# Kernel tuning notes

Hardware: AMD Instinct MI355X
Metric: run time of the kernel (lower is better)

## Reference

```python
import jax, jax.numpy as jnp
import numpy as np

B, T, C, H = 16, 2048, 192, 64

def setup_inputs() -> dict:
    key = jax.random.key(0)
    k1, k2, k3, k4 = jax.random.split(key, 4)
    x = jax.random.normal(k1, (B, T, C), dtype=jnp.float32)
    Wq = jax.random.normal(k2, (C, H), dtype=jnp.float32) * (C ** -0.5)
    Wk = jax.random.normal(k3, (C, H), dtype=jnp.float32) * (C ** -0.5)
    Wv = jax.random.normal(k4, (C, H), dtype=jnp.float32) * (C ** -0.5)
    return {"x": x, "Wq": Wq, "Wk": Wk, "Wv": Wv}

def reference(x, Wq, Wk, Wv):
    # One head of causal self-attention (dropout in eval mode / identity).
    q = x @ Wq                       # [B, T, H]
    k = x @ Wk                       # [B, T, H]
    v = x @ Wv                       # [B, T, H]
    scale = q.shape[-1] ** -0.5
    wei = jnp.einsum('bth,bsh->bts', q, k) * scale   # [B, T, T]
    t = wei.shape[-1]
    causal = jnp.tril(jnp.ones((t, t), dtype=bool))  # tril mask
    wei = jnp.where(causal, wei, -jnp.inf)
    wei = jax.nn.softmax(wei, axis=-1)
    out = jnp.einsum('bts,bsh->bth', wei, v)         # [B, T, H]
    return out
```

## Files before the change

kernel.cpp:

```cpp
#include <hip/hip_runtime.h>

#define B 16
#define T 2048
#define C 192
#define H 64

typedef __bf16 bf16x8 __attribute__((ext_vector_type(8)));
typedef __bf16 bf16x4 __attribute__((ext_vector_type(4)));
typedef float  f32x4  __attribute__((ext_vector_type(4)));

#define MFMA(a, b, c) __builtin_amdgcn_mfma_f32_16x16x32_bf16(a, b, c, 0, 0, 0)

#define SM_BIAS 24.0f

__global__ __launch_bounds__(512) void qkv_mfma_kernel(
    const float* __restrict__ x,
    const float* __restrict__ Wq, const float* __restrict__ Wk,
    const float* __restrict__ Wv,
    __bf16* __restrict__ qb, __bf16* __restrict__ kb, __bf16* __restrict__ vt)
{
    __shared__ __bf16 Ws[192][200];
    __shared__ __bf16 tile[128][72];

    const int tid  = threadIdx.x;
    const int w    = tid >> 6;
    const int lid  = tid & 15;
    const int quad = (tid & 63) >> 4;
    const int m0   = blockIdx.x * 128 + w * 16;

    #pragma unroll
    for (int i = 0; i < 18; i++) {
        const int p = i * 512 + tid;
        const int m = p / 3072;
        const int r = p - m * 3072;
        const int k = r >> 4;
        const int nc4 = (r & 15) << 2;
        const float* W = (m == 0) ? Wq : (m == 1) ? Wk : Wv;
        const float4 v = *(const float4*)(W + k * H + nc4);
        const int n = m * 64 + nc4;
        Ws[n + 0][k] = (__bf16)v.x;
        Ws[n + 1][k] = (__bf16)v.y;
        Ws[n + 2][k] = (__bf16)v.z;
        Ws[n + 3][k] = (__bf16)v.w;
    }

    const float* xrow = x + (size_t)(m0 + lid) * C + quad * 8;
    bf16x8 af[6];
    #pragma unroll
    for (int kc = 0; kc < 6; kc++) {
        const float4 a0 = *(const float4*)(xrow + kc * 32);
        const float4 a1 = *(const float4*)(xrow + kc * 32 + 4);
        af[kc][0] = (__bf16)a0.x; af[kc][1] = (__bf16)a0.y;
        af[kc][2] = (__bf16)a0.z; af[kc][3] = (__bf16)a0.w;
        af[kc][4] = (__bf16)a1.x; af[kc][5] = (__bf16)a1.y;
        af[kc][6] = (__bf16)a1.z; af[kc][7] = (__bf16)a1.w;
    }
    __syncthreads();

    f32x4 acc[12] = {};
    #pragma unroll
    for (int kc = 0; kc < 6; kc++)
        #pragma unroll
        for (int nt = 0; nt < 12; nt++) {
            const bf16x8 bfr =
                *(const bf16x8*)&Ws[nt * 16 + lid][kc * 32 + quad * 8];
            acc[nt] = MFMA(af[kc], bfr, acc[nt]);
        }

    #pragma unroll
    for (int nt = 0; nt < 8; nt++) {
        const int n = nt * 16 + lid;
        __bf16* dst = (n < 64) ? qb : kb;
        const int col = n & 63;
        const float scale = (n < 64) ? 0.1803368801111204f : 1.0f;
        #pragma unroll
        for (int r = 0; r < 4; r++) {
            const int row = m0 + quad * 4 + r;
            dst[(size_t)row * H + col] = (__bf16)(acc[nt][r] * scale);
        }
    }

    #pragma unroll
    for (int nt = 8; nt < 12; nt++) {
        const int col = (nt - 8) * 16 + lid;
        #pragma unroll
        for (int r = 0; r < 4; r++)
            tile[w * 16 + quad * 4 + r][col] = (__bf16)(acc[nt][r]);
    }
    __syncthreads();

    const int bb = blockIdx.x >> 4;
    const int t0 = (blockIdx.x & 15) << 7;
    #pragma unroll
    for (int it = 0; it < 2; ++it) {
        const int q   = it * 512 + tid;
        const int h   = q >> 4;
        const int tl0 = (q & 15) * 8;
        bf16x8 d;
        #pragma unroll
        for (int j = 0; j < 8; j++) d[j] = tile[tl0 + j][h];
        *(bf16x8*)(vt + ((size_t)(bb * H + h)) * T + t0 + tl0) = d;
    }
}

__global__ __launch_bounds__(512, 2) void attn_kernel(
    const __bf16* __restrict__ qb,
    const __bf16* __restrict__ kb,
    const __bf16* __restrict__ vt,
    float* __restrict__ out)
{
    __shared__ __bf16 Kb[2][2][64][72];
    __shared__ __bf16 Vb[2][2][64][68];

    const int tid  = threadIdx.x;
    const int wv   = tid >> 6;
    const int grp  = wv >> 2;
    const int w    = wv & 3;
    const int lid  = tid & 15;
    const int quad = (tid & 63) >> 4;

    const int b   = blockIdx.x & 15;
    const int pr  = blockIdx.x >> 4;
    const int qtH = 31 - pr, qtL = pr;
    const int nchH = qtH + 1;
    const int ntot = 33;
    const size_t bbase = (size_t)b * T;

    const int qH = (qtH << 6) + w * 16;
    const int qL = (qtL << 6) + w * 16;

    const __bf16* qrH = qb + (bbase + qH + lid) * H + quad * 8;
    const bf16x8 qfH0 = *(const bf16x8*)(qrH);
    const bf16x8 qfH1 = *(const bf16x8*)(qrH + 32);
    const __bf16* qrL = qb + (bbase + qL + lid) * H + quad * 8;
    const bf16x8 qfL0 = *(const bf16x8*)(qrL);
    const bf16x8 qfL1 = *(const bf16x8*)(qrL + 32);

    const __bf16* kgb = kb + bbase * H;
    const __bf16* vgb = vt + (size_t)b * H * T;

    const int ra = tid >> 3, ca = (tid & 7) * 8;

    auto keyof = [&](int i) {
        if (i > ntot - 1) i = ntot - 1;
        return (i < nchH ? i : i - nchH) << 6;
    };

    bf16x8 kr[2], vr2[2];
    auto prefetch = [&](int s) {
        #pragma unroll
        for (int g = 0; g < 2; g++) {
            const int key0 = keyof(2 * s + g);
            kr[g]  = *(const bf16x8*)(kgb + (size_t)(key0 + ra) * H + ca);
            vr2[g] = *(const bf16x8*)(vgb + (size_t)ra * T + key0 + ca);
        }
    };

    f32x4 OH[4] = {}, OL[4] = {};
    float lsH = 0.f, lsL = 0.f;

    auto doChunk = [&](f32x4 (&O)[4], float& ls, bf16x8 cq0, bf16x8 cq1,
                       int cqw, int key0, int cur) {
        const __bf16 (*Kc)[72] = Kb[cur][grp];
        const __bf16 (*Vc)[68] = Vb[cur][grp];
        bf16x8 kf[8];
        #pragma unroll
        for (int j = 0; j < 4; j++) {
            kf[2*j]   = *(const bf16x8*)&Kc[j * 16 + lid][quad * 8];
            kf[2*j+1] = *(const bf16x8*)&Kc[j * 16 + lid][32 + quad * 8];
        }
        bf16x8 bv0[4], bv1[4];
        #pragma unroll
        for (int ht = 0; ht < 4; ht++) {
            const __bf16* vr_ = &Vc[ht * 16 + lid][quad * 4];
            ((bf16x4*)&bv0[ht])[0] = *(const bf16x4*)(vr_);
            ((bf16x4*)&bv0[ht])[1] = *(const bf16x4*)(vr_ + 16);
            ((bf16x4*)&bv1[ht])[0] = *(const bf16x4*)(vr_ + 32);
            ((bf16x4*)&bv1[ht])[1] = *(const bf16x4*)(vr_ + 48);
        }
        bf16x8 af0, af1;
        const bool boundary = (key0 + 63 > cqw);
        #pragma unroll
        for (int j = 0; j < 4; j++) {
            f32x4 sS = {-SM_BIAS, -SM_BIAS, -SM_BIAS, -SM_BIAS};
            sS = MFMA(kf[2*j], cq0, sS);
            sS = MFMA(kf[2*j+1], cq1, sS);
            if (boundary) {
                #pragma unroll
                for (int r = 0; r < 4; r++)
                    if (key0 + j * 16 + quad * 4 + r > cqw + lid) sS[r] = -1e30f;
            }
            #pragma unroll
            for (int r = 0; r < 4; r++) {
                const float p = __builtin_amdgcn_exp2f(sS[r]);
                ls += p;
                if      (j == 0) af0[r]     = (__bf16)p;
                else if (j == 1) af0[4 + r] = (__bf16)p;
                else if (j == 2) af1[r]     = (__bf16)p;
                else             af1[4 + r] = (__bf16)p;
            }
        }
        #pragma unroll
        for (int ht = 0; ht < 4; ht++) {
            O[ht] = MFMA(af0, bv0[ht], O[ht]);
            O[ht] = MFMA(af1, bv1[ht], O[ht]);
        }
    };

    prefetch(0);
    int cur = 0;
    for (int s = 0; s < 17; s++) {
        *(bf16x8*)&Kb[cur][0][ra][ca] = kr[0];
        *(bf16x8*)&Kb[cur][1][ra][ca] = kr[1];
        *(bf16x8*)&Vb[cur][0][ra][ca] = vr2[0];
        *(bf16x8*)&Vb[cur][1][ra][ca] = vr2[1];
        __syncthreads();
        if (s + 1 < 17) prefetch(s + 1);

        const int i = 2 * s + grp;
        if (i < ntot) {
            const bool heavy = (i < nchH);
            const int key0 = (heavy ? i : i - nchH) << 6;
            if (heavy) doChunk(OH, lsH, qfH0, qfH1, qH, key0, cur);
            else       doChunk(OL, lsL, qfL0, qfL1, qL, key0, cur);
        }
        cur ^= 1;
    }

    __syncthreads();
    float* sO = (float*)&Kb[0][0][0][0];
    float* sL = (float*)&Vb[0][0][0][0];

    float lh = lsH; lh += __shfl_xor(lh, 16, 64); lh += __shfl_xor(lh, 32, 64);
    float ll = lsL; ll += __shfl_xor(ll, 16, 64); ll += __shfl_xor(ll, 32, 64);

    if (grp == 1) {
        #pragma unroll
        for (int ht = 0; ht < 4; ht++)
            #pragma unroll
            for (int r = 0; r < 4; r++) {
                sO[((0 * 4 + w) * 16 + quad * 4 + r) * 64 + ht * 16 + lid] = OH[ht][r];
                sO[((1 * 4 + w) * 16 + quad * 4 + r) * 64 + ht * 16 + lid] = OL[ht][r];
            }
        if ((tid & 63) < 16) {
            sL[(0 * 4 + w) * 16 + lid] = lh;
            sL[(1 * 4 + w) * 16 + lid] = ll;
        }
    }
    __syncthreads();
    if (grp == 0) {
        lh += sL[(0 * 4 + w) * 16 + lid];
        ll += sL[(1 * 4 + w) * 16 + lid];
        #pragma unroll
        for (int ht = 0; ht < 4; ht++)
            #pragma unroll
            for (int r = 0; r < 4; r++) {
                const float LrH = __shfl(lh, quad * 4 + r, 16);
                const float vH = OH[ht][r]
                    + sO[((0 * 4 + w) * 16 + quad * 4 + r) * 64 + ht * 16 + lid];
                out[(bbase + qH + quad * 4 + r) * H + ht * 16 + lid] = vH / LrH;

                const float LrL = __shfl(ll, quad * 4 + r, 16);
                const float vL = OL[ht][r]
                    + sO[((1 * 4 + w) * 16 + quad * 4 + r) * 64 + ht * 16 + lid];
                out[(bbase + qL + quad * 4 + r) * H + ht * 16 + lid] = vL / LrL;
            }
    }
}

extern "C" void kernel_launch(void* const* d_in, const int* in_sizes, int n_in,
                              void* d_out, int out_size, void* d_ws, size_t ws_size,
                              hipStream_t stream)
{
    const float* x  = (const float*)d_in[0];
    const float* Wq = (const float*)d_in[1];
    const float* Wk = (const float*)d_in[2];
    const float* Wv = (const float*)d_in[3];

    const size_t BTH = (size_t)B * T * H;
    __bf16* qbuf = (__bf16*)d_ws;
    __bf16* kbuf = qbuf + BTH;
    __bf16* vtb  = kbuf + BTH;
    float* outp = (float*)d_out;

    qkv_mfma_kernel<<<B * T / 128, 512, 0, stream>>>(x, Wq, Wk, Wv,
                                                     qbuf, kbuf, vtb);
    attn_kernel<<<B * T / 128, 512, 0, stream>>>(qbuf, kbuf, vtb, outp);
}
```

Before: 103.8 us.

## Split attention block into four key-groups with two query tiles per wave

Each workgroup now has four wave-groups that each process a different key chunk per step, instead of two. Every wave handles 32 query rows (two 16-row tiles), so each K/V fragment read from LDS feeds twice as many MFMAs. This halves the number of pipeline steps and barriers and cuts LDS read traffic per FLOP. In exchange it uses double the LDS and more registers for accumulators, which may lower occupancy, and the final cross-group reduction through shared memory is larger.

```diff
diff --git a/kernel.cpp b/kernel.cpp
--- a/kernel.cpp
+++ b/kernel.cpp
@@ -103,19 +103,21 @@
     }
 }
 
+#define KB_E (64 * 72)
+#define VB_E (64 * 68)
+
 __global__ __launch_bounds__(512, 2) void attn_kernel(
     const __bf16* __restrict__ qb,
     const __bf16* __restrict__ kb,
     const __bf16* __restrict__ vt,
     float* __restrict__ out)
 {
-    __shared__ __bf16 Kb[2][2][64][72];
-    __shared__ __bf16 Vb[2][2][64][68];
+    __shared__ __align__(16) __bf16 smem[8 * KB_E + 8 * VB_E];
 
     const int tid  = threadIdx.x;
     const int wv   = tid >> 6;
-    const int grp  = wv >> 2;
-    const int w    = wv & 3;
+    const int grp  = wv >> 1;
+    const int w2   = wv & 1;
     const int lid  = tid & 15;
     const int quad = (tid & 63) >> 4;
 
@@ -124,146 +126,188 @@
     const int qtH = 31 - pr, qtL = pr;
     const int nchH = qtH + 1;
     const int ntot = 33;
+    const int nsteps = 9;
     const size_t bbase = (size_t)b * T;
 
-    const int qH = (qtH << 6) + w * 16;
-    const int qL = (qtL << 6) + w * 16;
-
-    const __bf16* qrH = qb + (bbase + qH + lid) * H + quad * 8;
-    const bf16x8 qfH0 = *(const bf16x8*)(qrH);
-    const bf16x8 qfH1 = *(const bf16x8*)(qrH + 32);
-    const __bf16* qrL = qb + (bbase + qL + lid) * H + quad * 8;
-    const bf16x8 qfL0 = *(const bf16x8*)(qrL);
-    const bf16x8 qfL1 = *(const bf16x8*)(qrL + 32);
+    const int qHb = (qtH << 6) + w2 * 32;
+    const int qLb = (qtL << 6) + w2 * 32;
+
+    const __bf16* qp;
+    qp = qb + (bbase + qHb + lid) * H + quad * 8;
+    const bf16x8 qfHa0 = *(const bf16x8*)(qp);
+    const bf16x8 qfHa1 = *(const bf16x8*)(qp + 32);
+    qp = qb + (bbase + qHb + 16 + lid) * H + quad * 8;
+    const bf16x8 qfHb0 = *(const bf16x8*)(qp);
+    const bf16x8 qfHb1 = *(const bf16x8*)(qp + 32);
+    qp = qb + (bbase + qLb + lid) * H + quad * 8;
+    const bf16x8 qfLa0 = *(const bf16x8*)(qp);
+    const bf16x8 qfLa1 = *(const bf16x8*)(qp + 32);
+    qp = qb + (bbase + qLb + 16 + lid) * H + quad * 8;
+    const bf16x8 qfLb0 = *(const bf16x8*)(qp);
+    const bf16x8 qfLb1 = *(const bf16x8*)(qp + 32);
 
     const __bf16* kgb = kb + bbase * H;
     const __bf16* vgb = vt + (size_t)b * H * T;
 
-    const int ra = tid >> 3, ca = (tid & 7) * 8;
+    const int gq = tid >> 7;
+    const int tt = tid & 127;
 
     auto keyof = [&](int i) {
         if (i > ntot - 1) i = ntot - 1;
         return (i < nchH ? i : i - nchH) << 6;
     };
 
-    bf16x8 kr[2], vr2[2];
+    bf16x8 kr[4], vrr[4];
     auto prefetch = [&](int s) {
-        #pragma unroll
-        for (int g = 0; g < 2; g++) {
-            const int key0 = keyof(2 * s + g);
-            kr[g]  = *(const bf16x8*)(kgb + (size_t)(key0 + ra) * H + ca);
-            vr2[g] = *(const bf16x8*)(vgb + (size_t)ra * T + key0 + ca);
+        const int key0 = keyof(4 * s + gq);
+        #pragma unroll
+        for (int i = 0; i < 4; i++) {
+            const int p = i * 128 + tt, r = p >> 3, c = (p & 7) * 8;
+            kr[i]  = *(const bf16x8*)(kgb + (size_t)(key0 + r) * H + c);
+            vrr[i] = *(const bf16x8*)(vgb + (size_t)r * T + key0 + c);
         }
     };
 
-    f32x4 OH[4] = {}, OL[4] = {};
-    float lsH = 0.f, lsL = 0.f;
-
-    auto doChunk = [&](f32x4 (&O)[4], float& ls, bf16x8 cq0, bf16x8 cq1,
-                       int cqw, int key0, int cur) {
-        const __bf16 (*Kc)[72] = Kb[cur][grp];
-        const __bf16 (*Vc)[68] = Vb[cur][grp];
-        bf16x8 kf[8];
+    f32x4 OHa[4] = {}, OHb[4] = {}, OLa[4] = {}, OLb[4] = {};
+    float lsHa = 0.f, lsHb = 0.f, lsLa = 0.f, lsLb = 0.f;
+
+    auto doChunk = [&](f32x4 (&OA)[4], f32x4 (&OB)[4], float& lA, float& lB,
+                       bf16x8 qa0, bf16x8 qa1, bf16x8 qb0_, bf16x8 qb1_,
+                       int qbase, int key0, int cur) {
+        const __bf16 (*Kc)[72] =
+            (const __bf16(*)[72])(smem + (cur * 4 + grp) * KB_E);
+        const __bf16 (*Vc)[68] =
+            (const __bf16(*)[68])(smem + 8 * KB_E + (cur * 4 + grp) * VB_E);
+        bf16x8 afa0, afa1, afb0, afb1;
+        const bool boundary = (key0 + 63 > qbase);
         #pragma unroll
         for (int j = 0; j < 4; j++) {
-            kf[2*j]   = *(const bf16x8*)&Kc[j * 16 + lid][quad * 8];
-            kf[2*j+1] = *(const bf16x8*)&Kc[j * 16 + lid][32 + quad * 8];
-        }
-        bf16x8 bv0[4], bv1[4];
-        #pragma unroll
-        for (int ht = 0; ht < 4; ht++) {
-            const __bf16* vr_ = &Vc[ht * 16 + lid][quad * 4];
-            ((bf16x4*)&bv0[ht])[0] = *(const bf16x4*)(vr_);
-            ((bf16x4*)&bv0[ht])[1] = *(const bf16x4*)(vr_ + 16);
-            ((bf16x4*)&bv1[ht])[0] = *(const bf16x4*)(vr_ + 32);
-            ((bf16x4*)&bv1[ht])[1] = *(const bf16x4*)(vr_ + 48);
-        }
-        bf16x8 af0, af1;
-        const bool boundary = (key0 + 63 > cqw);
-        #pragma unroll
-        for (int j = 0; j < 4; j++) {
-            f32x4 sS = {-SM_BIAS, -SM_BIAS, -SM_BIAS, -SM_BIAS};
-            sS = MFMA(kf[2*j], cq0, sS);
-            sS = MFMA(kf[2*j+1], cq1, sS);
+            const bf16x8 k0 = *(const bf16x8*)&Kc[j * 16 + lid][quad * 8];
+            const bf16x8 k1 = *(const bf16x8*)&Kc[j * 16 + lid][32 + quad * 8];
+            f32x4 sa = {-SM_BIAS, -SM_BIAS, -SM_BIAS, -SM_BIAS};
+            f32x4 sb = sa;
+            sa = MFMA(k0, qa0, sa);  sa = MFMA(k1, qa1, sa);
+            sb = MFMA(k0, qb0_, sb); sb = MFMA(k1, qb1_, sb);
             if (boundary) {
                 #pragma unroll
-                for (int r = 0; r < 4; r++)
-                    if (key0 + j * 16 + quad * 4 + r > cqw + lid) sS[r] = -1e30f;
+                for (int r = 0; r < 4; r++) {
+                    const int key = key0 + j * 16 + quad * 4 + r;
+                    if (key > qbase + lid)      sa[r] = -1e30f;
+                    if (key > qbase + 16 + lid) sb[r] = -1e30f;
+                }
             }
             #pragma unroll
             for (int r = 0; r < 4; r++) {
-                const float p = __builtin_amdgcn_exp2f(sS[r]);
-                ls += p;
-                if      (j == 0) af0[r]     = (__bf16)p;
-                else if (j == 1) af0[4 + r] = (__bf16)p;
-                else if (j == 2) af1[r]     = (__bf16)p;
-                else             af1[4 + r] = (__bf16)p;
+                const float pa = __builtin_amdgcn_exp2f(sa[r]);
+                const float pb = __builtin_amdgcn_exp2f(sb[r]);
+                lA += pa; lB += pb;
+                if      (j == 0) { afa0[r]     = (__bf16)pa; afb0[r]     = (__bf16)pb; }
+                else if (j == 1) { afa0[4 + r] = (__bf16)pa; afb0[4 + r] = (__bf16)pb; }
+                else if (j == 2) { afa1[r]     = (__bf16)pa; afb1[r]     = (__bf16)pb; }
+                else             { afa1[4 + r] = (__bf16)pa; afb1[4 + r] = (__bf16)pb; }
             }
         }
         #pragma unroll
         for (int ht = 0; ht < 4; ht++) {
-            O[ht] = MFMA(af0, bv0[ht], O[ht]);
-            O[ht] = MFMA(af1, bv1[ht], O[ht]);
+            const __bf16* vp = &Vc[ht * 16 + lid][quad * 4];
+            bf16x8 bv0, bv1;
+            ((bf16x4*)&bv0)[0] = *(const bf16x4*)(vp);
+            ((bf16x4*)&bv0)[1] = *(const bf16x4*)(vp + 16);
+            ((bf16x4*)&bv1)[0] = *(const bf16x4*)(vp + 32);
+            ((bf16x4*)&bv1)[1] = *(const bf16x4*)(vp + 48);
+            OA[ht] = MFMA(afa0, bv0, OA[ht]);
+            OA[ht] = MFMA(afa1, bv1, OA[ht]);
+            OB[ht] = MFMA(afb0, bv0, OB[ht]);
+            OB[ht] = MFMA(afb1, bv1, OB[ht]);
         }
     };
 
     prefetch(0);
     int cur = 0;
-    for (int s = 0; s < 17; s++) {
-        *(bf16x8*)&Kb[cur][0][ra][ca] = kr[0];
-        *(bf16x8*)&Kb[cur][1][ra][ca] = kr[1];
-        *(bf16x8*)&Vb[cur][0][ra][ca] = vr2[0];
-        *(bf16x8*)&Vb[cur][1][ra][ca] = vr2[1];
+    for (int s = 0; s < nsteps; s++) {
+        #pragma unroll
+        for (int i = 0; i < 4; i++) {
+            const int p = i * 128 + tt, r = p >> 3, c = (p & 7) * 8;
+            *(bf16x8*)(smem + (cur * 4 + gq) * KB_E + r * 72 + c) = kr[i];
+            *(bf16x8*)(smem + 8 * KB_E + (cur * 4 + gq) * VB_E + r * 68 + c) = vrr[i];
+        }
         __syncthreads();
-        if (s + 1 < 17) prefetch(s + 1);
-
-        const int i = 2 * s + grp;
+        if (s + 1 < nsteps) prefetch(s + 1);
+
+        const int i = 4 * s + grp;
         if (i < ntot) {
             const bool heavy = (i < nchH);
             const int key0 = (heavy ? i : i - nchH) << 6;
-            if (heavy) doChunk(OH, lsH, qfH0, qfH1, qH, key0, cur);
-            else       doChunk(OL, lsL, qfL0, qfL1, qL, key0, cur);
+            if (heavy) doChunk(OHa, OHb, lsHa, lsHb,
+                               qfHa0, qfHa1, qfHb0, qfHb1, qHb, key0, cur);
+            else       doChunk(OLa, OLb, lsLa, lsLb,
+                               qfLa0, qfLa1, qfLb0, qfLb1, qLb, key0, cur);
         }
         cur ^= 1;
     }
 
     __syncthreads();
-    float* sO = (float*)&Kb[0][0][0][0];
-    float* sL = (float*)&Vb[0][0][0][0];
-
-    float lh = lsH; lh += __shfl_xor(lh, 16, 64); lh += __shfl_xor(lh, 32, 64);
-    float ll = lsL; ll += __shfl_xor(ll, 16, 64); ll += __shfl_xor(ll, 32, 64);
-
-    if (grp == 1) {
+    float* sO = (float*)smem;
+    float* sL = sO + 3 * 2 * 64 * 64;
+
+    lsHa += __shfl_xor(lsHa, 16, 64); lsHa += __shfl_xor(lsHa, 32, 64);
+    lsHb += __shfl_xor(lsHb, 16, 64); lsHb += __shfl_xor(lsHb, 32, 64);
+    lsLa += __shfl_xor(lsLa, 16, 64); lsLa += __shfl_xor(lsLa, 32, 64);
+    lsLb += __shfl_xor(lsLb, 16, 64); lsLb += __shfl_xor(lsLb, 32, 64);
+
+    if (grp != 0) {
+        const int gg = grp - 1;
         #pragma unroll
         for (int ht = 0; ht < 4; ht++)
             #pragma unroll
             for (int r = 0; r < 4; r++) {
-                sO[((0 * 4 + w) * 16 + quad * 4 + r) * 64 + ht * 16 + lid] = OH[ht][r];
-                sO[((1 * 4 + w) * 16 + quad * 4 + r) * 64 + ht * 16 + lid] = OL[ht][r];
+                const int qa = w2 * 32 + quad * 4 + r;
+                const int hh = ht * 16 + lid;
+                sO[((gg * 2 + 0) * 64 + qa)      * 64 + hh] = OHa[ht][r];
+                sO[((gg * 2 + 0) * 64 + qa + 16) * 64 + hh] = OHb[ht][r];
+                sO[((gg * 2 + 1) * 64 + qa)      * 64 + hh] = OLa[ht][r];
+                sO[((gg * 2 + 1) * 64 + qa + 16) * 64 + hh] = OLb[ht][r];
             }
         if ((tid & 63) < 16) {
-            sL[(0 * 4 + w) * 16 + lid] = lh;
-            sL[(1 * 4 + w) * 16 + lid] = ll;
+            sL[(gg * 2 + 0) * 64 + w2 * 32 + lid]      = lsHa;
+            sL[(gg * 2 + 0) * 64 + w2 * 32 + 16 + lid] = lsHb;
+            sL[(gg * 2 + 1) * 64 + w2 * 32 + lid]      = lsLa;
+            sL[(gg * 2 + 1) * 64 + w2 * 32 + 16 + lid] = lsLb;
         }
     }
     __syncthreads();
     if (grp == 0) {
-        lh += sL[(0 * 4 + w) * 16 + lid];
-        ll += sL[(1 * 4 + w) * 16 + lid];
+        #pragma unroll
+        for (int gg = 0; gg < 3; gg++) {
+            lsHa += sL[(gg * 2 + 0) * 64 + w2 * 32 + lid];
+            lsHb += sL[(gg * 2 + 0) * 64 + w2 * 32 + 16 + lid];
+            lsLa += sL[(gg * 2 + 1) * 64 + w2 * 32 + lid];
+            lsLb += sL[(gg * 2 + 1) * 64 + w2 * 32 + 16 + lid];
+        }
         #pragma unroll
         for (int ht = 0; ht < 4; ht++)
             #pragma unroll
             for (int r = 0; r < 4; r++) {
-                const float LrH = __shfl(lh, quad * 4 + r, 16);
-                const float vH = OH[ht][r]
-                    + sO[((0 * 4 + w) * 16 + quad * 4 + r) * 64 + ht * 16 + lid];
-                out[(bbase + qH + quad * 4 + r) * H + ht * 16 + lid] = vH / LrH;
-
-                const float LrL = __shfl(ll, quad * 4 + r, 16);
-                const float vL = OL[ht][r]
-                    + sO[((1 * 4 + w) * 16 + quad * 4 + r) * 64 + ht * 16 + lid];
-                out[(bbase + qL + quad * 4 + r) * H + ht * 16 + lid] = vL / LrL;
+                const int qa = w2 * 32 + quad * 4 + r;
+                const int hh = ht * 16 + lid;
+                float vHa = OHa[ht][r], vHb = OHb[ht][r];
+                float vLa = OLa[ht][r], vLb = OLb[ht][r];
+                #pragma unroll
+                for (int gg = 0; gg < 3; gg++) {
+                    vHa += sO[((gg * 2 + 0) * 64 + qa)      * 64 + hh];
+                    vHb += sO[((gg * 2 + 0) * 64 + qa + 16) * 64 + hh];
+                    vLa += sO[((gg * 2 + 1) * 64 + qa)      * 64 + hh];
+                    vLb += sO[((gg * 2 + 1) * 64 + qa + 16) * 64 + hh];
+                }
+                const float LHa = __shfl(lsHa, quad * 4 + r, 16);
+                const float LHb = __shfl(lsHb, quad * 4 + r, 16);
+                const float LLa = __shfl(lsLa, quad * 4 + r, 16);
+                const float LLb = __shfl(lsLb, quad * 4 + r, 16);
+                const int tH = (qtH << 6), tL = (qtL << 6);
+                out[(bbase + tH + qa)      * H + hh] = vHa / LHa;
+                out[(bbase + tH + qa + 16) * H + hh] = vHb / LHb;
+                out[(bbase + tL + qa)      * H + hh] = vLa / LLa;
+                out[(bbase + tL + qa + 16) * H + hh] = vLb / LLb;
             }
     }
 }
```

Result: slower. 106.2 us (+2.3%).
